# Performance work log

Hardware: AMD Instinct MI355X
Metric: run time of the kernel (lower is better)

The kernel has to match this reference:

```python
import jax, jax.numpy as jnp
import numpy as np

B, T, LMAX = 8, 4000, 2048
VOCAB, D, H = 20000, 128, 128
SCALE = float(H) ** 0.5  # torch uses pow(hidden_dim, 0.5) with hidden_dim=128 even though feature dim is 256


def setup_inputs() -> dict:
    key = jax.random.key(0)
    ks = jax.random.split(key, 22)
    def n(k, sh, s=0.05):
        return jax.random.normal(k, sh, dtype=jnp.float32) * s
    token_ids = jax.random.randint(ks[0], (B, T), 0, VOCAB)
    lens = jax.random.randint(ks[1], (B,), LMAX // 4, LMAX).at[0].set(LMAX)
    return dict(
        token_ids=token_ids, lens=lens,
        embed=n(ks[2], (VOCAB, D)),
        gru_wih0=n(ks[3], (2, 3 * H, D)), gru_whh0=n(ks[4], (2, 3 * H, H)),
        gru_bih0=n(ks[5], (2, 3 * H)), gru_bhh0=n(ks[6], (2, 3 * H)),
        gru_wih1=n(ks[7], (2, 3 * H, 2 * H)), gru_whh1=n(ks[8], (2, 3 * H, H)),
        gru_bih1=n(ks[9], (2, 3 * H)), gru_bhh1=n(ks[10], (2, 3 * H)),
        conv_w=n(ks[11], (3, D, D, 2)), conv_b=n(ks[12], (3, D)),
        Wa_w=n(ks[13], (2 * H, 4 * H)), Wa_b=n(ks[14], (2 * H,)),
        VT_w=n(ks[15], (1, 2 * H)), VT_b=n(ks[16], (1,)),
        Qw=n(ks[17], (2 * H, 2 * H)), Kw=n(ks[18], (2 * H, 2 * H)), Vw=n(ks[19], (2 * H, 2 * H)),
        fc_w=n(ks[20], (6, 2 * H)), fc_b=n(ks[21], (6,)),
    )


def _gru_dir(x, mask, Wih, Whh, bih, bhh):
    # One direction of a torch GRU layer with packed-sequence semantics:
    # outputs are zero past each sample's length; state frozen there.
    xg = jnp.einsum('bld,gd->blg', x, Wih) + bih   # [B, L, 3H] precomputed input gates
    xg = jnp.swapaxes(xg, 0, 1)                    # [L, B, 3H]
    m = jnp.swapaxes(mask, 0, 1)                   # [L, B]
    h0 = jnp.zeros((x.shape[0], H), x.dtype)

    def step(h, inp):
        g, mt = inp
        hh = h @ Whh.T + bhh
        r = jax.nn.sigmoid(g[:, :H] + hh[:, :H])
        z = jax.nn.sigmoid(g[:, H:2 * H] + hh[:, H:2 * H])
        nn_ = jnp.tanh(g[:, 2 * H:] + r * hh[:, 2 * H:])
        hn = (1.0 - z) * nn_ + z * h
        h2 = jnp.where(mt[:, None] > 0, hn, h)
        return h2, hn * mt[:, None]

    _, out = jax.lax.scan(step, h0, (xg, m))
    return jnp.swapaxes(out, 0, 1)                 # [B, L, H]


def _bi_gru_layer(x, mask, rev_idx, wih, whh, bih, bhh):
    out_f = _gru_dir(x, mask, wih[0], whh[0], bih[0], bhh[0])
    # packed bi-GRU: backward direction runs over each sample's reversed VALID segment
    xr = jnp.take_along_axis(x, rev_idx[:, :, None], axis=1)
    out_b = _gru_dir(xr, mask, wih[1], whh[1], bih[1], bhh[1])
    out_b = jnp.take_along_axis(out_b, rev_idx[:, :, None], axis=1) * mask[:, :, None]
    return jnp.concatenate([out_f, out_b], axis=-1)


def _additive_attn(s, enc, mask, Wa_w, Wa_b, VT_w, VT_b):
    sb = jnp.broadcast_to(s, enc.shape)
    x = jnp.concatenate([sb, enc], axis=-1)                     # [B, L, 4H]
    sh = jnp.tanh(jnp.einsum('blk,hk->blh', x, Wa_w) + Wa_b)
    res = jnp.einsum('blh,oh->blo', sh, VT_w)[..., 0] + VT_b[0]  # [B, L]
    # torch multiplies scores by 0/1 mask BEFORE softmax (pads get score 0, not -inf)
    w = jax.nn.softmax(res * mask, axis=-1)
    return jnp.sum(enc * w[..., None], axis=1, keepdims=True)   # [B, 1, 2H]


def _forward(embed, gru_wih0, gru_whh0, gru_bih0, gru_bhh0, gru_wih1, gru_whh1, gru_bih1, gru_bhh1,
             conv_w, conv_b, Wa_w, Wa_b, VT_w, VT_b, Qw, Kw, Vw, fc_w, fc_b, token_ids, lens):
    emb = embed[token_ids]                                      # [B, T, D]
    tpos = jnp.arange(LMAX)
    mask = (tpos[None, :] < lens[:, None]).astype(emb.dtype)    # [B, LMAX]
    rev_idx = jnp.where(tpos[None, :] < lens[:, None], lens[:, None] - 1 - tpos[None, :], tpos[None, :])
    pad_data = emb[:, :LMAX] * mask[..., None]                  # pad_packed_sequence zeroes pads

    # conv backbone runs on the FULL 4000-length padded embedding (as in torch), then trimmed/masked
    x = jnp.swapaxes(emb, 1, 2)                                 # [B, D, T]
    for i in range(3):
        x = jax.lax.conv_general_dilated(x, conv_w[i], (1,), 'VALID',
                                         dimension_numbers=('NCH', 'OIH', 'NCH'))
        x = jax.nn.relu(x + conv_b[i][None, :, None])
    conv_out = jnp.swapaxes(x, 1, 2)[:, :LMAX] * mask[..., None]  # [B, LMAX, D]

    h1 = _bi_gru_layer(pad_data, mask, rev_idx, gru_wih0, gru_whh0, gru_bih0, gru_bhh0)
    enc = _bi_gru_layer(h1, mask, rev_idx, gru_wih1, gru_whh1, gru_bih1, gru_bhh1)  # [B, LMAX, 2H]

    tmean = jnp.mean(conv_out, axis=1)                          # mean over padded length, as torch
    s = jnp.repeat(tmean, 2, axis=-1)[:, None, :]               # expand+reshape => interleaved duplicate [B,1,2H]

    inp2 = jnp.concatenate([pad_data, pad_data], axis=-1)       # [B, LMAX, 2H]
    Q = inp2 @ Qw.T
    K = inp2 @ Kw.T
    V = inp2 @ Vw.T
    scores = jnp.einsum('bqd,bkd->bqk', Q, K) / SCALE
    W = jax.nn.softmax(scores, axis=0)                          # torch F.softmax implicit dim -> 0 for 3D input
    W = W * mask[:, :, None]                                    # mask broadcast over key axis (query rows masked)
    Z = jnp.einsum('bqk,bkd->bqd', W, V)
    sa = jnp.sum(Z, axis=1, keepdims=True)                      # [B, 1, 2H]

    d1 = _additive_attn(s, enc, mask, Wa_w, Wa_b, VT_w, VT_b)
    d2 = _additive_attn(sa, enc, mask, Wa_w, Wa_b, VT_w, VT_b)
    dinput = 0.5 * (d1 + d2)                                    # mean over the concat dim
    return dinput @ fc_w.T + fc_b                               # [B, 1, 6]


def reference(token_ids, lens, embed, gru_wih0, gru_whh0, gru_bih0, gru_bhh0, gru_wih1, gru_whh1,
              gru_bih1, gru_bhh1, conv_w, conv_b, Wa_w, Wa_b, VT_w, VT_b, Qw, Kw, Vw, fc_w, fc_b):
    return _forward(embed, gru_wih0, gru_whh0, gru_bih0, gru_bhh0, gru_wih1, gru_whh1, gru_bih1,
                    gru_bhh1, conv_w, conv_b, Wa_w, Wa_b, VT_w, VT_b, Qw, Kw, Vw, fc_w, fc_b,
                    token_ids, lens)
```

## Files before the change

### kernel.cpp

```cpp
#include <hip/hip_runtime.h>
#include <stdint.h>

typedef unsigned short u16;
typedef unsigned int u32;
typedef __attribute__((ext_vector_type(8))) short short8;
typedef __attribute__((ext_vector_type(8))) u16 u16x8;
typedef __attribute__((ext_vector_type(4))) float f32x4;
typedef __attribute__((ext_vector_type(2))) float f32x2;
typedef __attribute__((ext_vector_type(2))) u32 u32x2;

#define DEVINL static __device__ __forceinline__

#if !__has_builtin(__builtin_amdgcn_exp2f)
#define __builtin_amdgcn_exp2f(x) exp2f(x)
#endif
#if !__has_builtin(__builtin_amdgcn_rcpf)
#define __builtin_amdgcn_rcpf(x) (1.0f/(x))
#endif

#define MFMA16(a, b, c) __builtin_amdgcn_mfma_f32_16x16x32_bf16((a), (b), (c), 0, 0, 0)

constexpr float LOG2E_C    = 1.4426950408889634f;
constexpr float TWOLOG2E_C = 2.8853900817779268f;
constexpr float RSCALE_LG  = 1.4426950408889634f / 11.313708498984761f;

constexpr size_t A256(size_t x){ return (x + 255) & ~(size_t)255; }
constexpr size_t OFS_EMB   = 0;
constexpr size_t OFS_PAD   = A256(OFS_EMB  + (size_t)8*2051*128*2);
constexpr size_t OFS_X1    = A256(OFS_PAD  + (size_t)8*2048*128*2);
constexpr size_t OFS_X2    = A256(OFS_X1   + (size_t)8*2050*128*2);
constexpr size_t OFS_QKVW  = A256(OFS_X2   + (size_t)8*2049*128*2);
constexpr size_t OFS_WA2   = A256(OFS_QKVW + (size_t)3*256*128*2);
constexpr size_t OFS_CONVW = A256(OFS_WA2  + (size_t)256*256*2);
constexpr size_t OFS_WIH0  = A256(OFS_CONVW+ (size_t)3*128*256*2);
constexpr size_t OFS_WIH1  = A256(OFS_WIH0 + (size_t)2*384*128*2);
constexpr size_t OFS_BIASX = A256(OFS_WIH1 + (size_t)2*384*256*2);
constexpr size_t OFS_BHHN  = A256(OFS_BIASX+ (size_t)2*2*384*4);
constexpr size_t OFS_Q     = A256(OFS_BHHN + (size_t)2*2*128*4);
constexpr size_t OFS_K     = A256(OFS_Q    + (size_t)8*2048*256*2);
constexpr size_t OFS_V     = A256(OFS_K    + (size_t)8*2048*256*2);
constexpr size_t OFS_CS    = A256(OFS_V    + (size_t)8*2048*256*2);
constexpr size_t OFS_TM    = A256(OFS_CS   + (size_t)8*2048*4);
constexpr size_t OFS_XG    = A256(OFS_TM   + (size_t)8*128*4);
constexpr size_t OFS_H1    = A256(OFS_XG   + (size_t)2*2048*8*384*4);
constexpr size_t OFS_ENC   = A256(OFS_H1   + (size_t)8*2048*256*2);
constexpr size_t OFS_ENCW  = A256(OFS_ENC  + (size_t)8*2048*256*2);
constexpr size_t OFS_SA    = A256(OFS_ENCW + (size_t)8*2048*256*4);
constexpr size_t OFS_RES   = A256(OFS_SA   + (size_t)8*256*4);
constexpr size_t OFS_DV    = A256(OFS_RES  + (size_t)8*2*2048*4);

DEVINL u16 f2bf(float f){
  u32 u = __builtin_bit_cast(u32, f);
  u32 r = (u + 0x7FFFu + ((u >> 16) & 1u)) >> 16;
  return (u16)r;
}
DEVINL float bf2f(u16 s){ return __builtin_bit_cast(float, (u32)s << 16); }

DEVINL short8 ld8cvt(const float* p, float sc){
  short8 o;
#pragma unroll
  for (int e = 0; e < 8; ++e) o[e] = (short)f2bf(p[e]*sc);
  return o;
}

DEVINL u32 cvtpk(float lo, float hi){
  u32 r;
  asm("v_cvt_pk_bf16_f32 %0, %1, %2" : "=v"(r) : "v"(lo), "v"(hi));
  return r;
}

DEVINL float sel4(const f32x4 v, int rr){
  float a = (rr & 1) ? v[1] : v[0];
  float bq = (rr & 1) ? v[3] : v[2];
  return (rr & 2) ? bq : a;
}

__global__ __launch_bounds__(256) void k_prep(
    const int* tok, const int* lens, const float* embed,
    const float* wih0, const float* wih1,
    const float* bih0, const float* bhh0, const float* bih1, const float* bhh1,
    const float* convw, const float* WaW, const float* Qw, const float* Kw, const float* Vw,
    char* ws)
{
  u16* emb_bf   = (u16*)(ws + OFS_EMB);
  u16* pad_bf   = (u16*)(ws + OFS_PAD);
  u16* qkvw     = (u16*)(ws + OFS_QKVW);
  u16* wa2      = (u16*)(ws + OFS_WA2);
  u16* convw_bf = (u16*)(ws + OFS_CONVW);
  u16* wih0_bf  = (u16*)(ws + OFS_WIH0);
  u16* wih1_bf  = (u16*)(ws + OFS_WIH1);
  float* biasx  = (float*)(ws + OFS_BIASX);
  float* bhhn   = (float*)(ws + OFS_BHHN);
  float* colsum = (float*)(ws + OFS_CS);
  float* tmean  = (float*)(ws + OFS_TM);
  float* dvec   = (float*)(ws + OFS_DV);
  const int S0 = 8*2051*128, S1 = 8*2048*128, S2 = 3*256*128, S3 = 256*256, S4 = 3*128*256;
  const int S5 = 2*384*128, S6 = 2*384*256, S7 = 2*2*384 + 2*2*128;
  const int S8 = 8*2048 + 8*128 + 8*2*256;
  const int TOT = S0+S1+S2+S3+S4+S5+S6+S7+S8;
  for (int i = blockIdx.x*256 + threadIdx.x; i < TOT; i += gridDim.x*256){
    int j = i;
    if (j < S0){
      int b = j / (2051*128); int r = j - b*(2051*128); int t = r >> 7, dd = r & 127;
      emb_bf[j] = f2bf(embed[(size_t)tok[b*4000 + t]*128 + dd]);
      continue;
    }
    j -= S0;
    if (j < S1){
      int b = j >> 18; int r = j & 262143; int t = r >> 7, dd = r & 127;
      float v = (t < lens[b]) ? embed[(size_t)tok[b*4000 + t]*128 + dd] : 0.f;
      pad_bf[j] = f2bf(v); continue;
    }
    j -= S1;
    if (j < S2){
      int z = j >> 15; int r = j & 32767; int o = r >> 7, k2 = r & 127;
      const float* W = (z == 0) ? Qw : (z == 1) ? Kw : Vw;
      qkvw[j] = f2bf(W[o*256 + k2] + W[o*256 + 128 + k2]); continue;
    }
    j -= S2;
    if (j < S3){ int h = j >> 8, k2 = j & 255; wa2[j] = f2bf(WaW[(size_t)h*512 + 256 + k2]); continue; }
    j -= S3;
    if (j < S4){
      int ly = j >> 15; int r = j & 32767; int o = r >> 8, k2 = r & 255;
      int i2 = k2 & 127, kap = k2 >> 7;
      convw_bf[j] = f2bf(convw[((size_t)(ly*128 + o)*128 + i2)*2 + kap]); continue;
    }
    j -= S4;
    if (j < S5){ wih0_bf[j] = f2bf(wih0[j]); continue; }
    j -= S5;
    if (j < S6){ wih1_bf[j] = f2bf(wih1[j]); continue; }
    j -= S6;
    if (j < S7){
      if (j < 1536){
        int ly = j / 768; int r = j - ly*768; int d = r / 384, g = r % 384;
        float bi = (ly ? bih1 : bih0)[d*384 + g];
        float bh = (ly ? bhh1 : bhh0)[d*384 + g];
        biasx[j] = (g < 256) ? (-LOG2E_C*(bi + bh)) : (TWOLOG2E_C*bi);
      } else {
        int j2 = j - 1536; int ly = j2 >> 8; int r = j2 & 255; int d = r >> 7, jj = r & 127;
        bhhn[j2] = TWOLOG2E_C*((ly ? bhh1 : bhh0)[d*384 + 256 + jj]);
      }
      continue;
    }
    j -= S7;
    if (j < 8*2048){ colsum[j] = 0.f; continue; }
    j -= 8*2048;
    if (j < 8*128){ tmean[j] = 0.f; continue; }
    dvec[j - 8*128] = 0.f;
  }
}

template<int KIN>
__global__ __launch_bounds__(256, 1) void k_xg(const int* lens, char* ws){
  const int tt = blockIdx.x, b = blockIdx.y, dir = blockIdx.z;
  constexpr int LAYER = (KIN == 128) ? 0 : 1;
  const u16* in = (KIN == 128) ? (const u16*)(ws + OFS_PAD) : (const u16*)(ws + OFS_H1);
  const u16* wmat = ((KIN == 128) ? (const u16*)(ws + OFS_WIH0) : (const u16*)(ws + OFS_WIH1))
                    + (size_t)dir*384*KIN;
  const float* biasx = (const float*)(ws + OFS_BIASX) + (LAYER*2 + dir)*384;
  float* xg = (float*)(ws + OFS_XG) + (size_t)dir*2048*3072;
  const int lenb = lens[b];
  __shared__ __align__(16) u16 sA[64][KIN + 8];
  constexpr int CH = KIN/8;
  const int tid = threadIdx.x, w = tid >> 6, l = tid & 63, rowg = l >> 4, cl = l & 15;
  for (int idx = tid; idx < 64*CH; idx += 256){
    int row = idx / CH, chn = idx % CH;
    int t = tt*64 + row;
    int tr = dir ? ((t < lenb) ? (lenb - 1 - t) : t) : t;
    *(u16x8*)&sA[row][chn*8] = *(const u16x8*)(in + ((size_t)(b*2048 + tr))*KIN + chn*8);
  }
  __syncthreads();
  f32x4 acc[24];
#pragma unroll
  for (int nt = 0; nt < 24; ++nt) acc[nt] = f32x4{0.f,0.f,0.f,0.f};
#pragma unroll
  for (int kk = 0; kk < KIN/32; ++kk){
    short8 a = *(const short8*)&sA[w*16 + cl][kk*32 + rowg*8];
#pragma unroll
    for (int nt = 0; nt < 24; ++nt){
      short8 bb = *(const short8*)(wmat + (size_t)(nt*16 + cl)*KIN + kk*32 + rowg*8);
      acc[nt] = MFMA16(a, bb, acc[nt]);
    }
  }
#pragma unroll
  for (int nt = 0; nt < 24; ++nt){
    const int g = nt*16 + cl;
    const float bx = biasx[g];
    const float sc = (nt < 16) ? -LOG2E_C : TWOLOG2E_C;
#pragma unroll
    for (int r = 0; r < 4; ++r){
      const int t = tt*64 + w*16 + rowg*4 + r;
      xg[((size_t)t*8 + b)*384 + g] = sc*acc[nt][r] + bx;
    }
  }
}

DEVINL void rec_block(char* smem, const float* xg_all, const float* whh_all,
    const float* bhhn_all, const int* lens, u16* out, int dir, int b)
{
  const float* xg  = xg_all + (size_t)dir*2048*3072 + b*384;
  const float* whh = whh_all + (size_t)dir*384*128;
  const float* bnd = bhhn_all + dir*128;
  const int tid = threadIdx.x;
  const int u = tid >> 6, l = tid & 63;
  const int c = l & 15, q = l >> 4;
  const int rsel = c & 3;
  const int j = u*16 + q*4 + rsel;
  const bool writer = (c < 4);
  const bool dirb = (dir != 0);
  const int lenb = lens[b];

  u16 (*hbuf)[128] = (u16(*)[128])smem;
  if (tid < 256) (&hbuf[0][0])[tid] = 0;

  short8 aR[4], aZ[4], aN[4];
#pragma unroll
  for (int kk = 0; kk < 4; ++kk){
    int k0 = kk*32 + q*8;
    int row = u*16 + c;
    aR[kk] = ld8cvt(whh + (size_t)(row)*128 + k0, -LOG2E_C);
    aZ[kk] = ld8cvt(whh + (size_t)(128 + row)*128 + k0, -LOG2E_C);
    aN[kk] = ld8cvt(whh + (size_t)(256 + row)*128 + k0, TWOLOG2E_C);
  }
  f32x4 bnU;
#pragma unroll
  for (int r = 0; r < 4; ++r) bnU[r] = bnd[u*16 + q*4 + r];

  const int offR = u*16 + q*4;
  const int offXN = 256 + j;
  u16* outp = out + (size_t)b*2048*256 + dir*128 + j;
  float hp = 0.f;

#define LOAD_STAGE(T_, Rv, Zv, Xn) do {              \
    const float* pb_ = xg + (size_t)(T_)*3072;       \
    Rv = *(const f32x4*)(pb_ + offR);                \
    Zv = *(const f32x4*)(pb_ + offR + 128);          \
    Xn = pb_[offXN];                                 \
  } while (0)

#define REC_STEP(T_, PF_, CUR_, Rv, Zv, Xn) do {                                      \
    short8 bf0_ = *(const short8*)(&hbuf[CUR_][0] + (q*8 + 0*32));                    \
    short8 bf1_ = *(const short8*)(&hbuf[CUR_][0] + (q*8 + 1*32));                    \
    short8 bf2_ = *(const short8*)(&hbuf[CUR_][0] + (q*8 + 2*32));                    \
    short8 bf3_ = *(const short8*)(&hbuf[CUR_][0] + (q*8 + 3*32));                    \
    __builtin_amdgcn_s_setprio(1);                                                    \
    f32x4 cR_ = MFMA16(aR[0], bf0_, Rv);                                              \
    f32x4 cZ_ = MFMA16(aZ[0], bf0_, Zv);                                              \
    f32x4 cN_ = MFMA16(aN[0], bf0_, bnU);                                             \
    const float* pfb_ = xg + (size_t)(PF_)*3072;                                      \
    Rv = *(const f32x4*)(pfb_ + offR);                                                \
    Zv = *(const f32x4*)(pfb_ + offR + 128);                                          \
    float Xnew_ = pfb_[offXN];                                                        \
    cR_ = MFMA16(aR[1], bf1_, cR_);                                                   \
    cZ_ = MFMA16(aZ[1], bf1_, cZ_);                                                   \
    cN_ = MFMA16(aN[1], bf1_, cN_);                                                   \
    cR_ = MFMA16(aR[2], bf2_, cR_);                                                   \
    cZ_ = MFMA16(aZ[2], bf2_, cZ_);                                                   \
    cN_ = MFMA16(aN[2], bf2_, cN_);                                                   \
    cR_ = MFMA16(aR[3], bf3_, cR_);                                                   \
    cZ_ = MFMA16(aZ[3], bf3_, cZ_);                                                   \
    cN_ = MFMA16(aN[3], bf3_, cN_);                                                   \
    __builtin_amdgcn_s_setprio(0);                                                    \
    const bool v_ = (T_) < lenb;                                                      \
    float gR = sel4(cR_, rsel);                                                       \
    float gZ = sel4(cZ_, rsel);                                                       \
    float gN = sel4(cN_, rsel);                                                       \
    float Rg = __builtin_amdgcn_rcpf(1.f + __builtin_amdgcn_exp2f(gR));               \
    float Zg = __builtin_amdgcn_rcpf(1.f + __builtin_amdgcn_exp2f(gZ));               \
    float y  = Xn + Rg*gN;                                                            \
    float NN = 1.f - 2.f*__builtin_amdgcn_rcpf(1.f + __builtin_amdgcn_exp2f(y));      \
    float hn = NN + Zg*(hp - NN);                                                     \
    hp = hn;                                                                          \
    Xn = Xnew_;                                                                       \
    u32 pk_ = cvtpk(hn, hn);                                                          \
    if (writer){                                                                      \
      hbuf[(CUR_) ^ 1][j] = (u16)pk_;                                                 \
      int to_ = dirb ? (v_ ? (lenb - 1 - (T_)) : (T_)) : (T_);                        \
      outp[(size_t)to_*256] = v_ ? (u16)pk_ : (u16)0;                                 \
    }                                                                                 \
    asm volatile("s_waitcnt lgkmcnt(0)" ::: "memory");                                \
    __builtin_amdgcn_s_barrier();                                                     \
  } while (0)

  f32x4 R0v, Z0v; float X0;
  f32x4 R1v, Z1v; float X1;
  f32x4 R2v, Z2v; float X2;
  f32x4 R3v, Z3v; float X3;
  __syncthreads();
  LOAD_STAGE(0, R0v, Z0v, X0);
  LOAD_STAGE(1, R1v, Z1v, X1);
  LOAD_STAGE(2, R2v, Z2v, X2);
  LOAD_STAGE(3, R3v, Z3v, X3);
  for (int t = 0; t < 2048; t += 4){
    int p4 = (t + 4 < 2048) ? (t + 4) : 2047;
    int p5 = (t + 5 < 2048) ? (t + 5) : 2047;
    int p6 = (t + 6 < 2048) ? (t + 6) : 2047;
    int p7 = (t + 7 < 2048) ? (t + 7) : 2047;
    REC_STEP(t + 0, p4, 0, R0v, Z0v, X0);
    REC_STEP(t + 1, p5, 1, R1v, Z1v, X1);
    REC_STEP(t + 2, p6, 0, R2v, Z2v, X2);
    REC_STEP(t + 3, p7, 1, R3v, Z3v, X3);
  }
#undef LOAD_STAGE
#undef REC_STEP
}

DEVINL void qkv_role(char* smem, char* ws, int tt, int b, int z){
  const u16* in = (const u16*)(ws + OFS_PAD);
  const u16* wmat = (const u16*)(ws + OFS_QKVW) + (size_t)z*256*128;
  u16* out = (u16*)(ws + ((z == 0) ? OFS_Q : (z == 1) ? OFS_K : OFS_V));
  u16 (*sA)[136] = (u16(*)[136])smem;
  const int tid = threadIdx.x;
  if (tid < 256){
    for (int idx = tid; idx < 64*16; idx += 256){
      int row = idx >> 4, chn = idx & 15;
      int t = tt*64 + row;
      *(u16x8*)&sA[row][chn*8] = *(const u16x8*)(in + ((size_t)(b*2048 + t))*128 + chn*8);
    }
  }
  __syncthreads();
  if (tid < 256){
    const int w = tid >> 6, l = tid & 63, rowg = l >> 4, cl = l & 15;
    f32x4 acc[16];
#pragma unroll
    for (int nt = 0; nt < 16; ++nt) acc[nt] = f32x4{0.f,0.f,0.f,0.f};
#pragma unroll
    for (int kk = 0; kk < 4; ++kk){
      short8 a = *(const short8*)&sA[w*16 + cl][kk*32 + rowg*8];
#pragma unroll
      for (int nt = 0; nt < 16; ++nt){
        short8 bb = *(const short8*)(wmat + (size_t)(nt*16 + cl)*128 + kk*32 + rowg*8);
        acc[nt] = MFMA16(a, bb, acc[nt]);
      }
    }
#pragma unroll
    for (int nt = 0; nt < 16; ++nt){
      int o = nt*16 + cl;
#pragma unroll
      for (int r = 0; r < 4; ++r){
        int t = tt*64 + w*16 + rowg*4 + r;
        out[((size_t)(b*2048 + t))*256 + o] = f2bf(acc[nt][r]);
      }
    }
  }
}

DEVINL void conv_layer_pass(u16 (*bi)[136], u16 (*bo)[136], const u16* wm, const float* bias,
                            int OUT_R, int w, int rowg, int cl){
#pragma unroll
  for (int pass = 0; pass < 2; ++pass){
    if (pass == 1 && !(w == 0 && OUT_R > 64)) break;
    const int rt = (pass == 0) ? w : 4;
    f32x4 acc[8];
#pragma unroll
    for (int nt = 0; nt < 8; ++nt) acc[nt] = f32x4{0.f,0.f,0.f,0.f};
#pragma unroll
    for (int kk = 0; kk < 8; ++kk){
      const int rofs = (kk >= 4) ? 1 : 0;
      short8 a = *(const short8*)&bi[rt*16 + cl + rofs][(kk & 3)*32 + rowg*8];
#pragma unroll
      for (int nt = 0; nt < 8; ++nt){
        short8 bb = *(const short8*)(wm + (size_t)(nt*16 + cl)*256 + kk*32 + rowg*8);
        acc[nt] = MFMA16(a, bb, acc[nt]);
      }
    }
#pragma unroll
    for (int nt = 0; nt < 8; ++nt){
      int o = nt*16 + cl;
      float bv = bias[o];
#pragma unroll
      for (int r = 0; r < 4; ++r){
        int ro = rt*16 + rowg*4 + r;
        if (ro < OUT_R) bo[ro][o] = f2bf(fmaxf(acc[nt][r] + bv, 0.f));
      }
    }
  }
}

DEVINL void conv_role(char* smem, const int* lens, const float* convb, char* ws, int tt, int b){
  const u16* emb = (const u16*)(ws + OFS_EMB);
  const u16* cw  = (const u16*)(ws + OFS_CONVW);
  float* tmean = (float*)(ws + OFS_TM);
  u16 (*bufA)[136] = (u16(*)[136])smem;
  u16 (*bufB)[136] = (u16(*)[136])(smem + 82*136*2);
  const int tid = threadIdx.x;
  const int w = tid >> 6, l = tid & 63, rowg = l >> 4, cl = l & 15;
  if (tid < 256){
    for (int idx = tid; idx < 67*16; idx += 256){
      int row = idx >> 4, chn = idx & 15;
      *(u16x8*)&bufA[row][chn*8] = *(const u16x8*)(emb + ((size_t)(b*2051 + tt*64 + row))*128 + chn*8);
    }
  }
  __syncthreads();
  if (tid < 256) conv_layer_pass(bufA, bufB, cw + (size_t)0*128*256, convb + 0,   66, w, rowg, cl);
  __syncthreads();
  if (tid < 256) conv_layer_pass(bufB, bufA, cw + (size_t)1*128*256, convb + 128, 65, w, rowg, cl);
  __syncthreads();
  if (tid < 256){
    const int lenb = lens[b];
    const u16* wm = cw + (size_t)2*128*256;
    f32x4 acc[8];
#pragma unroll
    for (int nt = 0; nt < 8; ++nt) acc[nt] = f32x4{0.f,0.f,0.f,0.f};
#pragma unroll
    for (int kk = 0; kk < 8; ++kk){
      const int rofs = (kk >= 4) ? 1 : 0;
      short8 a = *(const short8*)&bufA[w*16 + cl + rofs][(kk & 3)*32 + rowg*8];
#pragma unroll
      for (int nt = 0; nt < 8; ++nt){
        short8 bb = *(const short8*)(wm + (size_t)(nt*16 + cl)*256 + kk*32 + rowg*8);
        acc[nt] = MFMA16(a, bb, acc[nt]);
      }
    }
#pragma unroll
    for (int nt = 0; nt < 8; ++nt){
      int o = nt*16 + cl;
      float bias = convb[2*128 + o];
      float s = 0.f;
#pragma unroll
      for (int r = 0; r < 4; ++r){
        int t = tt*64 + w*16 + rowg*4 + r;
        if (t < lenb) s += fmaxf(acc[nt][r] + bias, 0.f);
      }
      s += __shfl_xor(s, 16); s += __shfl_xor(s, 32);
      if (l < 16) atomicAdd(&tmean[b*128 + o], s);
    }
  }
}

DEVINL void scores_role(char* smem, const int* lens, char* ws, int kt, int qt){
  const u16* Qp = (const u16*)(ws + OFS_Q);
  const u16* Kp = (const u16*)(ws + OFS_K);
  float* colsum = (float*)(ws + OFS_CS);
  u16 (*sQ)[264] = (u16(*)[264])smem;
  u16 (*sK)[264] = (u16(*)[264])(smem + 64*264*2);
  float (*cbuf)[64] = (float(*)[64])(smem + 2*64*264*2);
  const int tid = threadIdx.x, w = tid >> 6, l = tid & 63, rowg = l >> 4, cl = l & 15;
  if (tid < 256)
    for (int i = tid; i < 512; i += 256) cbuf[i >> 6][i & 63] = 0.f;
  f32x4 c[8][4];
#pragma unroll
  for (int b = 0; b < 8; ++b)
#pragma unroll
    for (int nt = 0; nt < 4; ++nt) c[b][nt] = f32x4{0.f,0.f,0.f,0.f};
#pragma unroll
  for (int b = 0; b < 8; ++b){
    __syncthreads();
    if (tid < 256){
      for (int idx = tid; idx < 4096; idx += 256){
        int which = idx >> 11, row = (idx >> 5) & 63, ch = idx & 31;
        if (which){
          *(u16x8*)&sK[row][ch*8] = *(const u16x8*)(Kp + ((size_t)(b*2048 + kt*64 + row))*256 + ch*8);
        } else {
          *(u16x8*)&sQ[row][ch*8] = *(const u16x8*)(Qp + ((size_t)(b*2048 + qt*64 + row))*256 + ch*8);
        }
      }
    }
    __syncthreads();
    if (tid < 256){
#pragma unroll
      for (int kk = 0; kk < 8; ++kk){
        short8 a = *(const short8*)&sQ[w*16 + cl][kk*32 + rowg*8];
#pragma unroll
        for (int nt = 0; nt < 4; ++nt){
          short8 bb = *(const short8*)&sK[nt*16 + cl][kk*32 + rowg*8];
          c[b][nt] = MFMA16(a, bb, c[b][nt]);
        }
      }
    }
  }
  if (tid < 256){
    int lenv[8];
#pragma unroll
    for (int b = 0; b < 8; ++b) lenv[b] = lens[b];
    const int q0 = qt*64 + w*16 + rowg*4;
    float cs[8][4];
#pragma unroll
    for (int b = 0; b < 8; ++b)
#pragma unroll
      for (int nt = 0; nt < 4; ++nt) cs[b][nt] = 0.f;
#pragma unroll
    for (int nt = 0; nt < 4; ++nt){
#pragma unroll
      for (int r = 0; r < 4; ++r){
        float m = c[0][nt][r];
#pragma unroll
        for (int b = 1; b < 8; ++b) m = fmaxf(m, c[b][nt][r]);
        float e[8], s = 0.f;
#pragma unroll
        for (int b = 0; b < 8; ++b){ e[b] = __builtin_amdgcn_exp2f((c[b][nt][r] - m)*RSCALE_LG); s += e[b]; }
        float ri = __builtin_amdgcn_rcpf(s);
#pragma unroll
        for (int b = 0; b < 8; ++b)
          if (q0 + r < lenv[b]) cs[b][nt] += e[b]*ri;
      }
    }
#pragma unroll
    for (int b = 0; b < 8; ++b)
#pragma unroll
      for (int nt = 0; nt < 4; ++nt){
        float v = cs[b][nt];
        v += __shfl_xor(v, 16); v += __shfl_xor(v, 32);
        if (l < 16) atomicAdd(&cbuf[b][nt*16 + l], v);
      }
  }
  __syncthreads();
  if (tid < 256){
    for (int i = tid; i < 512; i += 256)
      atomicAdd(&colsum[(size_t)(i >> 6)*2048 + kt*64 + (i & 63)], cbuf[i >> 6][i & 63]);
  }
}

__global__ __launch_bounds__(512, 2) void k_fusedA(const int* lens, const float* convb, char* ws,
    const float* whh0, u16* outH1)
{
  __shared__ __align__(16) char smem[90112];
  const int bid = blockIdx.x;
  if (bid < 16){
    rec_block(smem, (const float*)(ws + OFS_XG), whh0, (const float*)(ws + OFS_BHHN),
              lens, outH1, bid >> 3, bid & 7);
    return;
  }
  int r = bid - 16;
  if (r < 768){
    int z = r >> 8, rem = r & 255, b = rem >> 5, tt = rem & 31;
    qkv_role(smem, ws, tt, b, z);
    return;
  }
  r -= 768;
  conv_role(smem, lens, convb, ws, r & 31, r >> 5);
}

__global__ __launch_bounds__(512, 2) void k_fusedB(const int* lens, char* ws,
    const float* whh1, u16* outENC)
{
  __shared__ __align__(16) char smem[90112];
  const int bid = blockIdx.x;
  if (bid < 16){
    rec_block(smem, (const float*)(ws + OFS_XG), whh1, (const float*)(ws + OFS_BHHN) + 2*128,
              lens, outENC, bid >> 3, bid & 7);
    return;
  }
  int r = bid - 16;
  scores_role(smem, lens, ws, r & 31, r >> 5);
}

__global__ __launch_bounds__(256, 1) void k_tail1(char* ws){
  __shared__ __align__(16) u16 sA[64][264];
  const int bid = blockIdx.x;
  if (bid < 256){
    const int tt = bid & 31, b = bid >> 5;
    const u16* in = (const u16*)(ws + OFS_ENC);
    const u16* wmat = (const u16*)(ws + OFS_WA2);
    float* out = (float*)(ws + OFS_ENCW);
    const int tid = threadIdx.x, w = tid >> 6, l = tid & 63, rowg = l >> 4, cl = l & 15;
    for (int idx = tid; idx < 64*32; idx += 256){
      int row = idx >> 5, chn = idx & 31;
      int t = tt*64 + row;
      *(u16x8*)&sA[row][chn*8] = *(const u16x8*)(in + ((size_t)(b*2048 + t))*256 + chn*8);
    }
    __syncthreads();
    f32x4 acc[16];
#pragma unroll
    for (int nt = 0; nt < 16; ++nt) acc[nt] = f32x4{0.f,0.f,0.f,0.f};
#pragma unroll
    for (int kk = 0; kk < 8; ++kk){
      short8 a = *(const short8*)&sA[w*16 + cl][kk*32 + rowg*8];
#pragma unroll
      for (int nt = 0; nt < 16; ++nt){
        short8 bb = *(const short8*)(wmat + (size_t)(nt*16 + cl)*256 + kk*32 + rowg*8);
        acc[nt] = MFMA16(a, bb, acc[nt]);
      }
    }
#pragma unroll
    for (int nt = 0; nt < 16; ++nt){
      int h = nt*16 + cl;
#pragma unroll
      for (int r = 0; r < 4; ++r){
        int t = tt*64 + w*16 + rowg*4 + r;
        out[((size_t)(b*2048 + t))*256 + h] = acc[nt][r];
      }
    }
  } else {
    const int b = bid - 256, d = threadIdx.x;
    const float* cs = (const float*)(ws + OFS_CS) + (size_t)b*2048;
    const u16* V = (const u16*)(ws + OFS_V) + (size_t)b*2048*256;
    float a0 = 0.f, a1 = 0.f, a2 = 0.f, a3 = 0.f;
    for (int k = 0; k < 2048; k += 4){
      a0 += cs[k + 0]*bf2f(V[(size_t)(k + 0)*256 + d]);
      a1 += cs[k + 1]*bf2f(V[(size_t)(k + 1)*256 + d]);
      a2 += cs[k + 2]*bf2f(V[(size_t)(k + 2)*256 + d]);
      a3 += cs[k + 3]*bf2f(V[(size_t)(k + 3)*256 + d]);
    }
    ((float*)(ws + OFS_SA))[b*256 + d] = (a0 + a1) + (a2 + a3);
  }
}

__global__ __launch_bounds__(256) void k_res(const int* lens, const float* WaW, const float* Wab,
    const float* VTw, const float* VTb, char* ws){
  const int b = blockIdx.x, x = blockIdx.y, chb = blockIdx.z;
  const float* tm = (const float*)(ws + OFS_TM) + b*128;
  const float* sa = (const float*)(ws + OFS_SA) + b*256;
  const float* encW = (const float*)(ws + OFS_ENCW);
  float* res = (float*)(ws + OFS_RES) + ((size_t)b*2 + x)*2048;
  __shared__ float sw[256];
  __shared__ float vt[256];
  const int tid = threadIdx.x;
  {
    int h = tid;
    float acc = Wab[h];
    if (x == 0){
      for (int j = 0; j < 128; ++j)
        acc += tm[j]*(1.f/2048.f)*(WaW[(size_t)h*512 + 2*j] + WaW[(size_t)h*512 + 2*j + 1]);
    } else {
      for (int k = 0; k < 256; ++k) acc += sa[k]*WaW[(size_t)h*512 + k];
    }
    sw[h] = acc;
    vt[h] = VTw[h];
  }
  __syncthreads();
  const int lenb = lens[b];
  const int lsub = tid >> 2, q = tid & 3;
  const float vtb = VTb[0];
#pragma unroll
  for (int pass = 0; pass < 4; ++pass){
    const int ll = chb*256 + pass*64 + lsub;
    const float* er = encW + ((size_t)(b*2048 + ll))*256 + q*64;
    float racc = 0.f;
    for (int j = 0; j < 64; ++j){
      float u = er[j] + sw[q*64 + j];
      float th = 1.f - 2.f*__builtin_amdgcn_rcpf(1.f + __builtin_amdgcn_exp2f(u*TWOLOG2E_C));
      racc += th*vt[q*64 + j];
    }
    racc += __shfl_xor(racc, 1);
    racc += __shfl_xor(racc, 2);
    if (q == 0) res[ll] = (ll < lenb) ? (racc + vtb) : 0.f;
  }
}

__global__ __launch_bounds__(256) void k_attnfin(char* ws){
  const int b = blockIdx.x, x = blockIdx.y, ch = blockIdx.z;
  const float* res = (const float*)(ws + OFS_RES) + ((size_t)b*2 + x)*2048;
  const u16* enc = (const u16*)(ws + OFS_ENC);
  float* dvec = (float*)(ws + OFS_DV);
  __shared__ float sv[2048];
  __shared__ float red[8];
  const int tid = threadIdx.x;
  float m = -3.0e38f;
  for (int i = tid; i < 2048; i += 256){ float v = res[i]; sv[i] = v; m = fmaxf(m, v); }
#pragma unroll
  for (int o = 1; o < 64; o <<= 1) m = fmaxf(m, __shfl_xor(m, o));
  if ((tid & 63) == 0) red[tid >> 6] = m;
  __syncthreads();
  m = fmaxf(fmaxf(red[0], red[1]), fmaxf(red[2], red[3]));
  __syncthreads();
  float s = 0.f;
  for (int i = tid; i < 2048; i += 256){ float e = __builtin_amdgcn_exp2f((sv[i] - m)*LOG2E_C); sv[i] = e; s += e; }
#pragma unroll
  for (int o = 1; o < 64; o <<= 1) s += __shfl_xor(s, o);
  if ((tid & 63) == 0) red[tid >> 6] = s;
  __syncthreads();
  const float S = red[0] + red[1] + red[2] + red[3];
  const float ri = 1.0f/S;
  const int h = tid;
  const int l0b = ch*512;
  float a0 = 0.f, a1 = 0.f, a2 = 0.f, a3 = 0.f;
  for (int l0 = l0b; l0 < l0b + 512; l0 += 4){
    a0 += sv[l0 + 0]*bf2f(enc[((size_t)(b*2048 + l0 + 0))*256 + h]);
    a1 += sv[l0 + 1]*bf2f(enc[((size_t)(b*2048 + l0 + 1))*256 + h]);
    a2 += sv[l0 + 2]*bf2f(enc[((size_t)(b*2048 + l0 + 2))*256 + h]);
    a3 += sv[l0 + 3]*bf2f(enc[((size_t)(b*2048 + l0 + 3))*256 + h]);
  }
  atomicAdd(&dvec[((size_t)b*2 + x)*256 + h], ((a0 + a1) + (a2 + a3))*ri);
}

__global__ __launch_bounds__(64) void k_final(const float* fcw, const float* fcb, char* ws, float* outp){
  const int i = threadIdx.x;
  if (i >= 48) return;
  const int b = i/6, o = i%6;
  const float* dv = (const float*)(ws + OFS_DV);
  float acc = fcb[o];
  for (int h = 0; h < 256; ++h)
    acc += 0.5f*(dv[((size_t)b*2 + 0)*256 + h] + dv[((size_t)b*2 + 1)*256 + h])*fcw[o*256 + h];
  outp[i] = acc;
}

extern "C" void kernel_launch(void* const* d_in, const int* in_sizes, int n_in,
                              void* d_out, int out_size, void* d_ws, size_t ws_size,
                              hipStream_t stream)
{
  const int* tok    = (const int*)d_in[0];
  const int* lens   = (const int*)d_in[1];
  const float* embed= (const float*)d_in[2];
  const float* wih0 = (const float*)d_in[3];
  const float* whh0 = (const float*)d_in[4];
  const float* bih0 = (const float*)d_in[5];
  const float* bhh0 = (const float*)d_in[6];
  const float* wih1 = (const float*)d_in[7];
  const float* whh1 = (const float*)d_in[8];
  const float* bih1 = (const float*)d_in[9];
  const float* bhh1 = (const float*)d_in[10];
  const float* convw= (const float*)d_in[11];
  const float* convb= (const float*)d_in[12];
  const float* WaW  = (const float*)d_in[13];
  const float* Wab  = (const float*)d_in[14];
  const float* VTw  = (const float*)d_in[15];
  const float* VTb  = (const float*)d_in[16];
  const float* Qw   = (const float*)d_in[17];
  const float* Kw   = (const float*)d_in[18];
  const float* Vw   = (const float*)d_in[19];
  const float* fcw  = (const float*)d_in[20];
  const float* fcb  = (const float*)d_in[21];
  char* ws = (char*)d_ws;
  float* outp = (float*)d_out;

  hipLaunchKernelGGL(k_prep, dim3(2048), dim3(256), 0, stream,
      tok, lens, embed, wih0, wih1, bih0, bhh0, bih1, bhh1, convw, WaW, Qw, Kw, Vw, ws);
  hipLaunchKernelGGL((k_xg<128>), dim3(32,8,2), dim3(256), 0, stream, lens, ws);
  hipLaunchKernelGGL(k_fusedA, dim3(16 + 768 + 256), dim3(512), 0, stream,
      lens, convb, ws, whh0, (u16*)(ws + OFS_H1));
  hipLaunchKernelGGL((k_xg<256>), dim3(32,8,2), dim3(256), 0, stream, lens, ws);
  hipLaunchKernelGGL(k_fusedB, dim3(16 + 1024), dim3(512), 0, stream,
      lens, ws, whh1, (u16*)(ws + OFS_ENC));
  hipLaunchKernelGGL(k_tail1, dim3(264), dim3(256), 0, stream, ws);
  hipLaunchKernelGGL(k_res, dim3(8,2,8), dim3(256), 0, stream, lens, WaW, Wab, VTw, VTb, ws);
  hipLaunchKernelGGL(k_attnfin, dim3(8,2,4), dim3(256), 0, stream, ws);
  hipLaunchKernelGGL(k_final, dim3(1), dim3(64), 0, stream, fcw, fcb, ws, outp);
  (void)in_sizes; (void)n_in; (void)out_size; (void)ws_size;
}
```

Before: 1.739 ms.

## Fuse encoder projection with additive-attention scoring and vectorize prep conversions

The encoder-by-Wa matmul is now fused with the tanh/VT scoring step, so the fp32 projection no longer goes through a global ENCW buffer and the two attention query vectors are applied straight from MFMA accumulators. The self-attention sum is split across 64 blocks that combine with atomicAdd, which means the SA buffer is now zeroed in prep. The prep kernel converts 8 elements per thread with packed 16-byte stores and writes the embedding and padded copies in one pass. In exchange, each encres block recomputes both query projections (256x384 fp32 dot products), and the atomic accumulation makes the summation order nondeterministic.

```diff
diff --git a/kernel.cpp b/kernel.cpp
--- a/kernel.cpp
+++ b/kernel.cpp
@@ -94,43 +94,84 @@
   float* colsum = (float*)(ws + OFS_CS);
   float* tmean  = (float*)(ws + OFS_TM);
   float* dvec   = (float*)(ws + OFS_DV);
-  const int S0 = 8*2051*128, S1 = 8*2048*128, S2 = 3*256*128, S3 = 256*256, S4 = 3*128*256;
-  const int S5 = 2*384*128, S6 = 2*384*256, S7 = 2*2*384 + 2*2*128;
-  const int S8 = 8*2048 + 8*128 + 8*2*256;
-  const int TOT = S0+S1+S2+S3+S4+S5+S6+S7+S8;
+  float* sabuf  = (float*)(ws + OFS_SA);
+  const int V0 = 8*2051*16;
+  const int V1 = 3*256*16;
+  const int V2 = 256*32;
+  const int V3 = 3*128*32;
+  const int V4 = 2*384*16;
+  const int V5 = 2*384*32;
+  const int V6 = 2*2*384 + 2*2*128;
+  const int V7 = 8*2048 + 8*128 + 8*2*256 + 8*256;
+  const int TOT = V0+V1+V2+V3+V4+V5+V6+V7;
   for (int i = blockIdx.x*256 + threadIdx.x; i < TOT; i += gridDim.x*256){
     int j = i;
-    if (j < S0){
-      int b = j / (2051*128); int r = j - b*(2051*128); int t = r >> 7, dd = r & 127;
-      emb_bf[j] = f2bf(embed[(size_t)tok[b*4000 + t]*128 + dd]);
+    if (j < V0){
+      int b = j / (2051*16); int r = j - b*(2051*16); int t = r >> 4, chn = r & 15;
+      const float* ep = embed + (size_t)tok[b*4000 + t]*128 + chn*8;
+      u16x8 pk;
+#pragma unroll
+      for (int e = 0; e < 8; ++e) pk[e] = f2bf(ep[e]);
+      *(u16x8*)(emb_bf + ((size_t)(b*2051 + t))*128 + chn*8) = pk;
+      if (t < 2048){
+        u16x8 z = {0,0,0,0,0,0,0,0};
+        *(u16x8*)(pad_bf + ((size_t)(b*2048 + t))*128 + chn*8) = (t < lens[b]) ? pk : z;
+      }
       continue;
     }
-    j -= S0;
-    if (j < S1){
-      int b = j >> 18; int r = j & 262143; int t = r >> 7, dd = r & 127;
-      float v = (t < lens[b]) ? embed[(size_t)tok[b*4000 + t]*128 + dd] : 0.f;
-      pad_bf[j] = f2bf(v); continue;
-    }
-    j -= S1;
-    if (j < S2){
-      int z = j >> 15; int r = j & 32767; int o = r >> 7, k2 = r & 127;
+    j -= V0;
+    if (j < V1){
+      int z = j / (256*16); int r = j - z*(256*16); int o = r >> 4, chn = r & 15;
       const float* W = (z == 0) ? Qw : (z == 1) ? Kw : Vw;
-      qkvw[j] = f2bf(W[o*256 + k2] + W[o*256 + 128 + k2]); continue;
-    }
-    j -= S2;
-    if (j < S3){ int h = j >> 8, k2 = j & 255; wa2[j] = f2bf(WaW[(size_t)h*512 + 256 + k2]); continue; }
-    j -= S3;
-    if (j < S4){
-      int ly = j >> 15; int r = j & 32767; int o = r >> 8, k2 = r & 255;
-      int i2 = k2 & 127, kap = k2 >> 7;
-      convw_bf[j] = f2bf(convw[((size_t)(ly*128 + o)*128 + i2)*2 + kap]); continue;
-    }
-    j -= S4;
-    if (j < S5){ wih0_bf[j] = f2bf(wih0[j]); continue; }
-    j -= S5;
-    if (j < S6){ wih1_bf[j] = f2bf(wih1[j]); continue; }
-    j -= S6;
-    if (j < S7){
+      const float* p0 = W + (size_t)o*256 + chn*8;
+      u16x8 pk;
+#pragma unroll
+      for (int e = 0; e < 8; ++e) pk[e] = f2bf(p0[e] + p0[128 + e]);
+      *(u16x8*)(qkvw + ((size_t)z*256 + o)*128 + chn*8) = pk;
+      continue;
+    }
+    j -= V1;
+    if (j < V2){
+      int h = j >> 5, chn = j & 31;
+      const float* p = WaW + (size_t)h*512 + 256 + chn*8;
+      u16x8 pk;
+#pragma unroll
+      for (int e = 0; e < 8; ++e) pk[e] = f2bf(p[e]);
+      *(u16x8*)(wa2 + (size_t)h*256 + chn*8) = pk;
+      continue;
+    }
+    j -= V2;
+    if (j < V3){
+      int ly = j / (128*32); int r = j - ly*(128*32); int o = r >> 5, chn = r & 31;
+      u16x8 pk;
+#pragma unroll
+      for (int e = 0; e < 8; ++e){
+        int k2 = chn*8 + e; int i2 = k2 & 127, kap = k2 >> 7;
+        pk[e] = f2bf(convw[((size_t)(ly*128 + o)*128 + i2)*2 + kap]);
+      }
+      *(u16x8*)(convw_bf + ((size_t)(ly*128 + o))*256 + chn*8) = pk;
+      continue;
+    }
+    j -= V3;
+    if (j < V4){
+      const float* p = wih0 + (size_t)j*8;
+      u16x8 pk;
+#pragma unroll
+      for (int e = 0; e < 8; ++e) pk[e] = f2bf(p[e]);
+      *(u16x8*)(wih0_bf + (size_t)j*8) = pk;
+      continue;
+    }
+    j -= V4;
+    if (j < V5){
+      const float* p = wih1 + (size_t)j*8;
+      u16x8 pk;
+#pragma unroll
+      for (int e = 0; e < 8; ++e) pk[e] = f2bf(p[e]);
+      *(u16x8*)(wih1_bf + (size_t)j*8) = pk;
+      continue;
+    }
+    j -= V5;
+    if (j < V6){
       if (j < 1536){
         int ly = j / 768; int r = j - ly*768; int d = r / 384, g = r % 384;
         float bi = (ly ? bih1 : bih0)[d*384 + g];
@@ -142,11 +183,13 @@
       }
       continue;
     }
-    j -= S7;
+    j -= V6;
     if (j < 8*2048){ colsum[j] = 0.f; continue; }
     j -= 8*2048;
     if (j < 8*128){ tmean[j] = 0.f; continue; }
-    dvec[j - 8*128] = 0.f;
+    j -= 8*128;
+    if (j < 8*2*256){ dvec[j] = 0.f; continue; }
+    sabuf[j - 8*2*256] = 0.f;
   }
 }
 
@@ -545,96 +588,82 @@
   scores_role(smem, lens, ws, r & 31, r >> 5);
 }
 
-__global__ __launch_bounds__(256, 1) void k_tail1(char* ws){
-  __shared__ __align__(16) u16 sA[64][264];
-  const int bid = blockIdx.x;
-  if (bid < 256){
-    const int tt = bid & 31, b = bid >> 5;
-    const u16* in = (const u16*)(ws + OFS_ENC);
-    const u16* wmat = (const u16*)(ws + OFS_WA2);
-    float* out = (float*)(ws + OFS_ENCW);
-    const int tid = threadIdx.x, w = tid >> 6, l = tid & 63, rowg = l >> 4, cl = l & 15;
-    for (int idx = tid; idx < 64*32; idx += 256){
-      int row = idx >> 5, chn = idx & 31;
-      int t = tt*64 + row;
-      *(u16x8*)&sA[row][chn*8] = *(const u16x8*)(in + ((size_t)(b*2048 + t))*256 + chn*8);
-    }
-    __syncthreads();
-    f32x4 acc[16];
-#pragma unroll
-    for (int nt = 0; nt < 16; ++nt) acc[nt] = f32x4{0.f,0.f,0.f,0.f};
-#pragma unroll
-    for (int kk = 0; kk < 8; ++kk){
-      short8 a = *(const short8*)&sA[w*16 + cl][kk*32 + rowg*8];
-#pragma unroll
-      for (int nt = 0; nt < 16; ++nt){
-        short8 bb = *(const short8*)(wmat + (size_t)(nt*16 + cl)*256 + kk*32 + rowg*8);
-        acc[nt] = MFMA16(a, bb, acc[nt]);
-      }
-    }
-#pragma unroll
-    for (int nt = 0; nt < 16; ++nt){
-      int h = nt*16 + cl;
-#pragma unroll
-      for (int r = 0; r < 4; ++r){
-        int t = tt*64 + w*16 + rowg*4 + r;
-        out[((size_t)(b*2048 + t))*256 + h] = acc[nt][r];
-      }
-    }
-  } else {
-    const int b = bid - 256, d = threadIdx.x;
-    const float* cs = (const float*)(ws + OFS_CS) + (size_t)b*2048;
-    const u16* V = (const u16*)(ws + OFS_V) + (size_t)b*2048*256;
-    float a0 = 0.f, a1 = 0.f, a2 = 0.f, a3 = 0.f;
-    for (int k = 0; k < 2048; k += 4){
-      a0 += cs[k + 0]*bf2f(V[(size_t)(k + 0)*256 + d]);
-      a1 += cs[k + 1]*bf2f(V[(size_t)(k + 1)*256 + d]);
-      a2 += cs[k + 2]*bf2f(V[(size_t)(k + 2)*256 + d]);
-      a3 += cs[k + 3]*bf2f(V[(size_t)(k + 3)*256 + d]);
-    }
-    ((float*)(ws + OFS_SA))[b*256 + d] = (a0 + a1) + (a2 + a3);
-  }
-}
-
-__global__ __launch_bounds__(256) void k_res(const int* lens, const float* WaW, const float* Wab,
-    const float* VTw, const float* VTb, char* ws){
-  const int b = blockIdx.x, x = blockIdx.y, chb = blockIdx.z;
+__global__ __launch_bounds__(256) void k_sa(char* ws){
+  const int b = blockIdx.x >> 3, kc = blockIdx.x & 7;
+  const int d = threadIdx.x;
+  const float* cs = (const float*)(ws + OFS_CS) + (size_t)b*2048 + kc*256;
+  const u16* V = (const u16*)(ws + OFS_V) + ((size_t)(b*2048 + kc*256))*256;
+  float a0 = 0.f, a1 = 0.f, a2 = 0.f, a3 = 0.f;
+  for (int k = 0; k < 256; k += 4){
+    a0 += cs[k + 0]*bf2f(V[(size_t)(k + 0)*256 + d]);
+    a1 += cs[k + 1]*bf2f(V[(size_t)(k + 1)*256 + d]);
+    a2 += cs[k + 2]*bf2f(V[(size_t)(k + 2)*256 + d]);
+    a3 += cs[k + 3]*bf2f(V[(size_t)(k + 3)*256 + d]);
+  }
+  atomicAdd(&((float*)(ws + OFS_SA))[b*256 + d], (a0 + a1) + (a2 + a3));
+}
+
+__global__ __launch_bounds__(256, 1) void k_encres(const int* lens, const float* WaW,
+    const float* Wab, const float* VTw, const float* VTb, char* ws){
+  const int tt = blockIdx.x, b = blockIdx.y;
+  const u16* in = (const u16*)(ws + OFS_ENC);
+  const u16* wmat = (const u16*)(ws + OFS_WA2);
   const float* tm = (const float*)(ws + OFS_TM) + b*128;
   const float* sa = (const float*)(ws + OFS_SA) + b*256;
-  const float* encW = (const float*)(ws + OFS_ENCW);
-  float* res = (float*)(ws + OFS_RES) + ((size_t)b*2 + x)*2048;
-  __shared__ float sw[256];
+  float* res = (float*)(ws + OFS_RES);
+  __shared__ __align__(16) u16 sA[64][264];
+  __shared__ float sw[2][256];
   __shared__ float vt[256];
-  const int tid = threadIdx.x;
+  const int tid = threadIdx.x, w = tid >> 6, l = tid & 63, rowg = l >> 4, cl = l & 15;
   {
-    int h = tid;
-    float acc = Wab[h];
-    if (x == 0){
-      for (int j = 0; j < 128; ++j)
-        acc += tm[j]*(1.f/2048.f)*(WaW[(size_t)h*512 + 2*j] + WaW[(size_t)h*512 + 2*j + 1]);
-    } else {
-      for (int k = 0; k < 256; ++k) acc += sa[k]*WaW[(size_t)h*512 + k];
-    }
-    sw[h] = acc;
-    vt[h] = VTw[h];
-  }
-  __syncthreads();
+    const int h = tid;
+    float a0 = Wab[h], a1 = Wab[h];
+    const float* wr = WaW + (size_t)h*512;
+    for (int jj = 0; jj < 128; ++jj)
+      a0 += tm[jj]*(1.f/2048.f)*(wr[2*jj] + wr[2*jj + 1]);
+    for (int k = 0; k < 256; ++k) a1 += sa[k]*wr[k];
+    sw[0][h] = a0; sw[1][h] = a1; vt[h] = VTw[h];
+  }
+  for (int idx = tid; idx < 64*32; idx += 256){
+    int row = idx >> 5, chn = idx & 31;
+    int t = tt*64 + row;
+    *(u16x8*)&sA[row][chn*8] = *(const u16x8*)(in + ((size_t)(b*2048 + t))*256 + chn*8);
+  }
+  __syncthreads();
+  f32x4 acc[16];
+#pragma unroll
+  for (int nt = 0; nt < 16; ++nt) acc[nt] = f32x4{0.f,0.f,0.f,0.f};
+#pragma unroll
+  for (int kk = 0; kk < 8; ++kk){
+    short8 a = *(const short8*)&sA[w*16 + cl][kk*32 + rowg*8];
+#pragma unroll
+    for (int nt = 0; nt < 16; ++nt){
+      short8 bb = *(const short8*)(wmat + (size_t)(nt*16 + cl)*256 + kk*32 + rowg*8);
+      acc[nt] = MFMA16(a, bb, acc[nt]);
+    }
+  }
   const int lenb = lens[b];
-  const int lsub = tid >> 2, q = tid & 3;
   const float vtb = VTb[0];
 #pragma unroll
-  for (int pass = 0; pass < 4; ++pass){
-    const int ll = chb*256 + pass*64 + lsub;
-    const float* er = encW + ((size_t)(b*2048 + ll))*256 + q*64;
-    float racc = 0.f;
-    for (int j = 0; j < 64; ++j){
-      float u = er[j] + sw[q*64 + j];
-      float th = 1.f - 2.f*__builtin_amdgcn_rcpf(1.f + __builtin_amdgcn_exp2f(u*TWOLOG2E_C));
-      racc += th*vt[q*64 + j];
-    }
-    racc += __shfl_xor(racc, 1);
-    racc += __shfl_xor(racc, 2);
-    if (q == 0) res[ll] = (ll < lenb) ? (racc + vtb) : 0.f;
+  for (int x = 0; x < 2; ++x){
+#pragma unroll
+    for (int r = 0; r < 4; ++r){
+      float racc = 0.f;
+#pragma unroll
+      for (int nt = 0; nt < 16; ++nt){
+        float uarg = acc[nt][r] + sw[x][nt*16 + cl];
+        float th = 1.f - 2.f*__builtin_amdgcn_rcpf(1.f + __builtin_amdgcn_exp2f(uarg*TWOLOG2E_C));
+        racc += th*vt[nt*16 + cl];
+      }
+      racc += __shfl_xor(racc, 1);
+      racc += __shfl_xor(racc, 2);
+      racc += __shfl_xor(racc, 4);
+      racc += __shfl_xor(racc, 8);
+      if (cl == 0){
+        int row = tt*64 + w*16 + rowg*4 + r;
+        res[((size_t)b*2 + x)*2048 + row] = (row < lenb) ? (racc + vtb) : 0.f;
+      }
+    }
   }
 }
 
@@ -714,7 +743,7 @@
   char* ws = (char*)d_ws;
   float* outp = (float*)d_out;
 
-  hipLaunchKernelGGL(k_prep, dim3(2048), dim3(256), 0, stream,
+  hipLaunchKernelGGL(k_prep, dim3(1398), dim3(256), 0, stream,
       tok, lens, embed, wih0, wih1, bih0, bhh0, bih1, bhh1, convw, WaW, Qw, Kw, Vw, ws);
   hipLaunchKernelGGL((k_xg<128>), dim3(32,8,2), dim3(256), 0, stream, lens, ws);
   hipLaunchKernelGGL(k_fusedA, dim3(16 + 768 + 256), dim3(512), 0, stream,
@@ -722,8 +751,8 @@
   hipLaunchKernelGGL((k_xg<256>), dim3(32,8,2), dim3(256), 0, stream, lens, ws);
   hipLaunchKernelGGL(k_fusedB, dim3(16 + 1024), dim3(512), 0, stream,
       lens, ws, whh1, (u16*)(ws + OFS_ENC));
-  hipLaunchKernelGGL(k_tail1, dim3(264), dim3(256), 0, stream, ws);
-  hipLaunchKernelGGL(k_res, dim3(8,2,8), dim3(256), 0, stream, lens, WaW, Wab, VTw, VTb, ws);
+  hipLaunchKernelGGL(k_sa, dim3(64), dim3(256), 0, stream, ws);
+  hipLaunchKernelGGL(k_encres, dim3(32,8), dim3(256), 0, stream, lens, WaW, Wab, VTw, VTb, ws);
   hipLaunchKernelGGL(k_attnfin, dim3(8,2,4), dim3(256), 0, stream, ws);
   hipLaunchKernelGGL(k_final, dim3(1), dim3(64), 0, stream, fcw, fcb, ws, outp);
   (void)in_sizes; (void)n_in; (void)out_size; (void)ws_size;
```

Measured after the change: 1.708 ms. About the same (-1.8%).
